# Optimization experiments

Hardware: AMD Instinct MI355X
Metric: run time of the kernel (lower is better)

Reference implementation:

```python
import jax, jax.numpy as jnp
import numpy as np

N, E, IN, H, C = 50000, 800000, 128, 256, 2
EPS = 1e-5


def setup_inputs() -> dict:
    key = jax.random.key(0)
    ks = jax.random.split(key, 12)
    inp = {
        "x": jax.random.normal(ks[0], (N, IN), jnp.float32),
        "edge_index": jax.random.randint(ks[1], (2, E), 0, N, jnp.int32),
        "w_nei0": jax.random.normal(ks[2], (IN, H), jnp.float32) * 0.05,
        "w_root0": jax.random.normal(ks[3], (IN, H), jnp.float32) * 0.05,
        "b0": jnp.zeros((H,), jnp.float32),
        "w_nei": jax.random.normal(ks[4], (2, H, H), jnp.float32) * 0.05,
        "w_root": jax.random.normal(ks[5], (2, H, H), jnp.float32) * 0.05,
        "b": jnp.zeros((2, H), jnp.float32),
        "bn_gamma": jnp.ones((3, H), jnp.float32),
        "bn_beta": jnp.zeros((3, H), jnp.float32),
        "bn_mean": jax.random.normal(ks[6], (3, H), jnp.float32) * 0.05,
        "bn_var": jnp.ones((3, H), jnp.float32),
        "w1": jax.random.normal(ks[7], (H, H // 2), jnp.float32) * 0.05,
        "b1": jnp.zeros((H // 2,), jnp.float32),
        "w2": jax.random.normal(ks[8], (H // 2, C), jnp.float32) * 0.05,
        "b2": jnp.zeros((C,), jnp.float32),
    }
    return inp


def _mean_aggregate(h, src, dst, inv_deg):
    # gather source-node features, scatter-sum to destinations, divide by degree
    agg = jax.ops.segment_sum(h[src], dst, num_segments=N)  # (N, d)
    return agg * inv_deg[:, None]


def _forward(x, edge_index, w_nei0, w_root0, b0, w_nei, w_root, b,
             bn_gamma, bn_beta, bn_mean, bn_var, w1, b1, w2, b2):
    src, dst = edge_index[0], edge_index[1]
    deg = jax.ops.segment_sum(jnp.ones((E,), x.dtype), dst, num_segments=N)
    inv_deg = 1.0 / jnp.maximum(deg, 1.0)

    h = x
    wn_list = [w_nei0, w_nei[0], w_nei[1]]
    wr_list = [w_root0, w_root[0], w_root[1]]
    bias_list = [b0, b[0], b[1]]
    for i in range(3):
        mean_nb = _mean_aggregate(h, src, dst, inv_deg)          # (N, d_in)
        h = mean_nb @ wn_list[i] + bias_list[i] + h @ wr_list[i]  # SAGEConv
        # BatchNorm1d (eval: running stats) + ReLU; dropout is identity in eval
        h = (h - bn_mean[i]) * jax.lax.rsqrt(bn_var[i] + EPS) * bn_gamma[i] + bn_beta[i]
        h = jax.nn.relu(h)

    h = jax.nn.relu(h @ w1 + b1)
    logits = h @ w2 + b2
    return jax.nn.log_softmax(logits, axis=1)


def reference(x, edge_index, w_nei0, w_root0, b0, w_nei, w_root, b,
              bn_gamma, bn_beta, bn_mean, bn_var, w1, b1, w2, b2):
    return _forward(x, edge_index, w_nei0, w_root0, b0, w_nei, w_root, b,
                    bn_gamma, bn_beta, bn_mean, bn_var, w1, b1, w2, b2)
```

## Files before the change

### kernel.cpp

```cpp
#include <hip/hip_runtime.h>
#include <hip/hip_fp16.h>

#define N_NODES 50000
#define N_EDGES 800000
#define DIM_IN 128
#define DIM_H 256

typedef _Float16 f16;
typedef _Float16 half8 __attribute__((ext_vector_type(8)));
typedef _Float16 f16x4 __attribute__((ext_vector_type(4)));
typedef _Float16 f16x2 __attribute__((ext_vector_type(2)));
typedef float f32x4 __attribute__((ext_vector_type(4)));
typedef unsigned int u32;

__device__ __forceinline__ void gload_lds16(const void* g, void* l) {
    __builtin_amdgcn_global_load_lds(
        (const __attribute__((address_space(1))) u32*)g,
        (__attribute__((address_space(3))) u32*)l,
        16, 0, 0);
}


__global__ void k_deg(const int* __restrict__ dst, int* __restrict__ deg) {
    int i = blockIdx.x * 256 + threadIdx.x;
    if (i < N_EDGES) atomicAdd(&deg[dst[i]], 1);
}

__global__ void k_scan1(const int* __restrict__ deg, int* __restrict__ row_start,
                        int* __restrict__ partials) {
    __shared__ int sm[256];
    int t = threadIdx.x;
    int i = blockIdx.x * 256 + t;
    int v = (i < N_NODES) ? deg[i] : 0;
    sm[t] = v;
    __syncthreads();
    for (int ofs = 1; ofs < 256; ofs <<= 1) {
        int add = (t >= ofs) ? sm[t - ofs] : 0;
        __syncthreads();
        sm[t] += add;
        __syncthreads();
    }
    if (i < N_NODES) row_start[i] = sm[t] - v;
    if (t == 255) partials[blockIdx.x] = sm[255];
}

__global__ void k_scan2(const int* __restrict__ partials, int* __restrict__ pscan, int nblk) {
    __shared__ int sm[256];
    int t = threadIdx.x;
    int v = (t < nblk) ? partials[t] : 0;
    sm[t] = v;
    __syncthreads();
    for (int ofs = 1; ofs < 256; ofs <<= 1) {
        int add = (t >= ofs) ? sm[t - ofs] : 0;
        __syncthreads();
        sm[t] += add;
        __syncthreads();
    }
    pscan[t] = sm[t] - v;
}

__global__ void k_scan3(const int* __restrict__ deg, int* __restrict__ row_start,
                        const int* __restrict__ pscan, float* __restrict__ inv_deg) {
    int i = blockIdx.x * 256 + threadIdx.x;
    if (i < N_NODES) {
        row_start[i] += pscan[blockIdx.x];
        int d = deg[i];
        inv_deg[i] = 1.0f / (float)(d > 1 ? d : 1);
        if (i == 0) row_start[N_NODES] = N_EDGES;
    }
}

__global__ void k_fill(const int* __restrict__ src, const int* __restrict__ dst,
                       const int* __restrict__ row_start, int* __restrict__ cursor,
                       int* __restrict__ csr) {
    int i = blockIdx.x * 256 + threadIdx.x;
    if (i < N_EDGES) {
        int d = dst[i];
        int p = atomicAdd(&cursor[d], 1);
        csr[row_start[d] + p] = src[i];
    }
}


__global__ void k_cvt_x(const float* __restrict__ x, f16* __restrict__ o) {
    int i = blockIdx.x * 256 + threadIdx.x;
    if (i < N_NODES * DIM_IN / 4) {
        float4 v = ((const float4*)x)[i];
        f16x4 h = {(f16)v.x, (f16)v.y, (f16)v.z, (f16)v.w};
        *(f16x4*)(o + (size_t)i * 4) = h;
    }
}

__global__ void k_tcvt(const float* __restrict__ W, f16* __restrict__ Wt, int K, int NN) {
    int t = blockIdx.x * 256 + threadIdx.x;
    if (t < K * NN) {
        int n = t / K, k = t - n * K;
        Wt[t] = (f16)W[(size_t)k * NN + n];
    }
}

__global__ void k_st(const float* __restrict__ b0, const float* __restrict__ bvec,
                     const float* __restrict__ gamma, const float* __restrict__ beta,
                     const float* __restrict__ mean, const float* __restrict__ var,
                     const float* __restrict__ b1, float* __restrict__ st) {
    int c = threadIdx.x;
    for (int layer = 0; layer < 3; layer++) {
        float bias = (layer == 0) ? b0[c] : bvec[(layer - 1) * DIM_H + c];
        float g = gamma[layer * DIM_H + c];
        float be = beta[layer * DIM_H + c];
        float mu = mean[layer * DIM_H + c];
        float va = var[layer * DIM_H + c];
        float s = g * rsqrtf(va + 1e-5f);
        st[layer * 512 + c] = s;
        st[layer * 512 + 256 + c] = (bias - mu) * s + be;
    }
    st[3 * 512 + c] = 1.0f;
    st[3 * 512 + 256 + c] = (c < 128) ? b1[c] : 0.0f;
}


template <int D>
__global__ void k_agg(const f16* __restrict__ h, const int* __restrict__ row_start,
                      const int* __restrict__ csr, const float* __restrict__ inv_deg,
                      f16* __restrict__ agg) {
    constexpr int V = D / 64;
    typedef _Float16 fvec __attribute__((ext_vector_type(V)));
    int wid = threadIdx.x >> 6;
    int lane = threadIdx.x & 63;
    int v = blockIdx.x * 4 + wid;
    if (v >= N_NODES) return;
    int e0 = row_start[v], e1 = row_start[v + 1];
    float acc[V];
#pragma unroll
    for (int j = 0; j < V; j++) acc[j] = 0.0f;

    const int li = lane & 15;
    for (int e = e0; e < e1; e += 16) {
        int ee = e + li;
        int idx = csr[ee < e1 ? ee : e1 - 1];
        int rem = e1 - e;
        fvec hv[16];
#pragma unroll
        for (int j = 0; j < 16; j++) {
            int s = __shfl(idx, j);
            hv[j] = *(const fvec*)(h + (size_t)s * D + lane * V);
        }
#pragma unroll
        for (int j = 0; j < 16; j++) {
            if (j < rem) {
#pragma unroll
                for (int q = 0; q < V; q++) acc[q] += (float)hv[j][q];
            }
        }
    }

    float sc = inv_deg[v];
    fvec o;
#pragma unroll
    for (int j = 0; j < V; j++) o[j] = (f16)(acc[j] * sc);
    *(fvec*)(agg + (size_t)v * D + lane * V) = o;
}


__global__ __launch_bounds__(256) void k_gemm(
    const f16* __restrict__ A1, int lda1, const f16* __restrict__ B1, int k1,
    const f16* __restrict__ A2, int lda2, const f16* __restrict__ B2, int k2,
    const float* __restrict__ sc, const float* __restrict__ sh,
    f16* __restrict__ out, int ldo, int M) {
    __shared__ f16 aT[128 * 32];
    __shared__ f16 bT[128 * 32];
    const int tid = threadIdx.x;
    const int lane = tid & 63;
    const int wid = tid >> 6;
    const int wm = wid >> 1, wn = wid & 1;
    const int m0 = blockIdx.x * 128;
    const int n0 = blockIdx.y * 128;
    f32x4 acc[4][4] = {};

    const int srow = tid >> 2;
    const int schunk = (tid & 3) ^ ((tid >> 3) & 3);
    const int ktot = k1 + k2;

    for (int kk = 0; kk < ktot; kk += 32) {
        const f16 *Ap, *Bp;
        int lda, ldb, kloc;
        if (kk < k1) { Ap = A1; Bp = B1; lda = lda1; ldb = k1; kloc = kk; }
        else         { Ap = A2; Bp = B2; lda = lda2; ldb = k2; kloc = kk - k1; }
#pragma unroll
        for (int hh = 0; hh < 2; hh++) {
            int r = hh * 64 + srow;
            int gm = m0 + r;
            gm = gm < M ? gm : M - 1;
            gload_lds16(Ap + (size_t)gm * lda + kloc + schunk * 8,
                        (char*)aT + hh * 4096 + tid * 16);
            gload_lds16(Bp + (size_t)(n0 + r) * ldb + kloc + schunk * 8,
                        (char*)bT + hh * 4096 + tid * 16);
        }
        __syncthreads();
        half8 af[4], bf[4];
#pragma unroll
        for (int mi = 0; mi < 4; mi++) {
            int row = wm * 64 + mi * 16 + (lane & 15);
            int ch = (lane >> 4) ^ ((row >> 1) & 3);
            af[mi] = *(const half8*)((const char*)aT + row * 64 + ch * 16);
        }
#pragma unroll
        for (int ni = 0; ni < 4; ni++) {
            int row = wn * 64 + ni * 16 + (lane & 15);
            int ch = (lane >> 4) ^ ((row >> 1) & 3);
            bf[ni] = *(const half8*)((const char*)bT + row * 64 + ch * 16);
        }
#pragma unroll
        for (int mi = 0; mi < 4; mi++)
#pragma unroll
            for (int ni = 0; ni < 4; ni++)
                acc[mi][ni] = __builtin_amdgcn_mfma_f32_16x16x32_f16(af[mi], bf[ni],
                                                                     acc[mi][ni], 0, 0, 0);
        __syncthreads();
    }

#pragma unroll
    for (int mi = 0; mi < 4; mi++) {
#pragma unroll
        for (int ni = 0; ni < 4; ni++) {
            int gcol = n0 + wn * 64 + ni * 16 + (lane & 15);
            float s = sc[gcol], t = sh[gcol];
#pragma unroll
            for (int r = 0; r < 4; r++) {
                int grow = m0 + wm * 64 + mi * 16 + (lane >> 4) * 4 + r;
                if (grow < M) {
                    float val = fmaxf(acc[mi][ni][r] * s + t, 0.0f);
                    out[(size_t)grow * ldo + gcol] = (f16)val;
                }
            }
        }
    }
}


__global__ void k_head2(const f16* __restrict__ h4, const float* __restrict__ w2,
                        const float* __restrict__ b2, float* __restrict__ out) {
    int wid = threadIdx.x >> 6, lane = threadIdx.x & 63;
    int row = blockIdx.x * 4 + wid;
    if (row >= N_NODES) return;
    f16x2 hv = *(const f16x2*)(h4 + (size_t)row * 128 + lane * 2);
    float4 w = *(const float4*)(w2 + lane * 4);
    float p0 = (float)hv[0] * w.x + (float)hv[1] * w.z;
    float p1 = (float)hv[0] * w.y + (float)hv[1] * w.w;
    for (int o = 32; o > 0; o >>= 1) {
        p0 += __shfl_xor(p0, o);
        p1 += __shfl_xor(p1, o);
    }
    if (lane == 0) {
        float l0 = p0 + b2[0], l1 = p1 + b2[1];
        float m = fmaxf(l0, l1);
        float lse = m + logf(expf(l0 - m) + expf(l1 - m));
        out[(size_t)row * 2] = l0 - lse;
        out[(size_t)row * 2 + 1] = l1 - lse;
    }
}


extern "C" void kernel_launch(void* const* d_in, const int* in_sizes, int n_in,
                              void* d_out, int out_size, void* d_ws, size_t ws_size,
                              hipStream_t stream) {
    const float* x     = (const float*)d_in[0];
    const int*   ei    = (const int*)d_in[1];
    const float* wn0   = (const float*)d_in[2];
    const float* wr0   = (const float*)d_in[3];
    const float* b0    = (const float*)d_in[4];
    const float* wn12  = (const float*)d_in[5];
    const float* wr12  = (const float*)d_in[6];
    const float* bvec  = (const float*)d_in[7];
    const float* gamma = (const float*)d_in[8];
    const float* beta  = (const float*)d_in[9];
    const float* mean  = (const float*)d_in[10];
    const float* var   = (const float*)d_in[11];
    const float* w1    = (const float*)d_in[12];
    const float* b1    = (const float*)d_in[13];
    const float* w2    = (const float*)d_in[14];
    const float* b2    = (const float*)d_in[15];
    const int* srcv = ei;
    const int* dstv = ei + N_EDGES;

    char* p = (char*)d_ws;
    auto alloc = [&](size_t bytes) {
        char* r = p;
        p += (bytes + 255) & ~(size_t)255;
        return r;
    };
    int*   deg       = (int*)alloc((size_t)N_NODES * 4);
    int*   row_start = (int*)alloc((size_t)(N_NODES + 1) * 4);
    int*   cursor    = (int*)alloc((size_t)N_NODES * 4);
    float* inv_deg   = (float*)alloc((size_t)N_NODES * 4);
    int*   partials  = (int*)alloc(256 * 4);
    int*   pscan     = (int*)alloc(256 * 4);
    int*   csr       = (int*)alloc((size_t)N_EDGES * 4);
    f16*   Wn0t      = (f16*)alloc(128 * 256 * 2);
    f16*   Wr0t      = (f16*)alloc(128 * 256 * 2);
    f16*   Wn1t      = (f16*)alloc(256 * 256 * 2);
    f16*   Wr1t      = (f16*)alloc(256 * 256 * 2);
    f16*   Wn2t      = (f16*)alloc(256 * 256 * 2);
    f16*   Wr2t      = (f16*)alloc(256 * 256 * 2);
    f16*   W1t       = (f16*)alloc(256 * 128 * 2);
    float* st        = (float*)alloc(4 * 512 * 4);
    f16*   hA        = (f16*)alloc((size_t)N_NODES * 256 * 2);
    f16*   hB        = (f16*)alloc((size_t)N_NODES * 256 * 2);
    f16*   agg       = (f16*)alloc((size_t)N_NODES * 256 * 2);

    hipMemsetAsync(deg, 0, (size_t)N_NODES * 4, stream);
    hipMemsetAsync(cursor, 0, (size_t)N_NODES * 4, stream);

    const int EB = (N_EDGES + 255) / 256;
    const int NBLK = (N_NODES + 255) / 256;
    k_deg<<<EB, 256, 0, stream>>>(dstv, deg);
    k_scan1<<<NBLK, 256, 0, stream>>>(deg, row_start, partials);
    k_scan2<<<1, 256, 0, stream>>>(partials, pscan, NBLK);
    k_scan3<<<NBLK, 256, 0, stream>>>(deg, row_start, pscan, inv_deg);
    k_fill<<<EB, 256, 0, stream>>>(srcv, dstv, row_start, cursor, csr);

    k_cvt_x<<<(N_NODES * DIM_IN / 4 + 255) / 256, 256, 0, stream>>>(x, hA);
    k_tcvt<<<128, 256, 0, stream>>>(wn0, Wn0t, 128, 256);
    k_tcvt<<<128, 256, 0, stream>>>(wr0, Wr0t, 128, 256);
    k_tcvt<<<256, 256, 0, stream>>>(wn12, Wn1t, 256, 256);
    k_tcvt<<<256, 256, 0, stream>>>(wn12 + 65536, Wn2t, 256, 256);
    k_tcvt<<<256, 256, 0, stream>>>(wr12, Wr1t, 256, 256);
    k_tcvt<<<256, 256, 0, stream>>>(wr12 + 65536, Wr2t, 256, 256);
    k_tcvt<<<128, 256, 0, stream>>>(w1, W1t, 256, 128);
    k_st<<<1, 256, 0, stream>>>(b0, bvec, gamma, beta, mean, var, b1, st);

    const int AB = (N_NODES + 3) / 4;
    dim3 g2((N_NODES + 127) / 128, 2), g1((N_NODES + 127) / 128, 1);

    k_agg<128><<<AB, 256, 0, stream>>>(hA, row_start, csr, inv_deg, agg);
    k_gemm<<<g2, 256, 0, stream>>>(agg, 128, Wn0t, 128, hA, 128, Wr0t, 128,
                                   st + 0, st + 256, hB, 256, N_NODES);
    k_agg<256><<<AB, 256, 0, stream>>>(hB, row_start, csr, inv_deg, agg);
    k_gemm<<<g2, 256, 0, stream>>>(agg, 256, Wn1t, 256, hB, 256, Wr1t, 256,
                                   st + 512, st + 768, hA, 256, N_NODES);
    k_agg<256><<<AB, 256, 0, stream>>>(hA, row_start, csr, inv_deg, agg);
    k_gemm<<<g2, 256, 0, stream>>>(agg, 256, Wn2t, 256, hA, 256, Wr2t, 256,
                                   st + 1024, st + 1280, hB, 256, N_NODES);
    k_gemm<<<g1, 256, 0, stream>>>(hB, 256, W1t, 256, (const f16*)nullptr, 0,
                                   (const f16*)nullptr, 0,
                                   st + 1536, st + 1792, agg, 128, N_NODES);
    k_head2<<<AB, 256, 0, stream>>>(agg, w2, b2, (float*)d_out);
}
```

Baseline: 398.1 us.

## Double-buffer GEMM LDS tiles, split 256-wide aggregation across waves, fuse MLP head

The GEMM kernel now double-buffers its LDS tiles so the global-to-LDS load of the next K slice is issued before the MFMAs on the current slice. The 256-dim aggregation now gives each node two waves, each loading half the row as 4-byte vectors, which doubles the waves available for the gather but re-reads the CSR indices twice. The final W1 GEMM is fused with the W2 projection and log-softmax, removing an intermediate write/read and one launch. Doubling LDS per block may reduce occupancy.

```diff
diff --git a/kernel.cpp b/kernel.cpp
--- a/kernel.cpp
+++ b/kernel.cpp
@@ -119,46 +119,71 @@
 }
 
 
-template <int D>
-__global__ void k_agg(const f16* __restrict__ h, const int* __restrict__ row_start,
-                      const int* __restrict__ csr, const float* __restrict__ inv_deg,
-                      f16* __restrict__ agg) {
-    constexpr int V = D / 64;
-    typedef _Float16 fvec __attribute__((ext_vector_type(V)));
+__global__ void k_agg128(const f16* __restrict__ h, const int* __restrict__ row_start,
+                         const int* __restrict__ csr, const float* __restrict__ inv_deg,
+                         f16* __restrict__ agg) {
     int wid = threadIdx.x >> 6;
     int lane = threadIdx.x & 63;
     int v = blockIdx.x * 4 + wid;
     if (v >= N_NODES) return;
     int e0 = row_start[v], e1 = row_start[v + 1];
-    float acc[V];
-#pragma unroll
-    for (int j = 0; j < V; j++) acc[j] = 0.0f;
+    float acc[2] = {0.0f, 0.0f};
 
     const int li = lane & 15;
     for (int e = e0; e < e1; e += 16) {
         int ee = e + li;
         int idx = csr[ee < e1 ? ee : e1 - 1];
         int rem = e1 - e;
-        fvec hv[16];
+        f16x2 hv[16];
 #pragma unroll
         for (int j = 0; j < 16; j++) {
             int s = __shfl(idx, j);
-            hv[j] = *(const fvec*)(h + (size_t)s * D + lane * V);
+            hv[j] = *(const f16x2*)(h + (size_t)s * 128 + lane * 2);
         }
 #pragma unroll
         for (int j = 0; j < 16; j++) {
-            if (j < rem) {
-#pragma unroll
-                for (int q = 0; q < V; q++) acc[q] += (float)hv[j][q];
-            }
+            if (j < rem) { acc[0] += (float)hv[j][0]; acc[1] += (float)hv[j][1]; }
         }
     }
 
     float sc = inv_deg[v];
-    fvec o;
-#pragma unroll
-    for (int j = 0; j < V; j++) o[j] = (f16)(acc[j] * sc);
-    *(fvec*)(agg + (size_t)v * D + lane * V) = o;
+    f16x2 o = {(f16)(acc[0] * sc), (f16)(acc[1] * sc)};
+    *(f16x2*)(agg + (size_t)v * 128 + lane * 2) = o;
+}
+
+
+__global__ void k_agg256(const f16* __restrict__ h, const int* __restrict__ row_start,
+                         const int* __restrict__ csr, const float* __restrict__ inv_deg,
+                         f16* __restrict__ agg) {
+    int wid = threadIdx.x >> 6;
+    int lane = threadIdx.x & 63;
+    int v = blockIdx.x * 2 + (wid >> 1);
+    int half = wid & 1;
+    if (v >= N_NODES) return;
+    int e0 = row_start[v], e1 = row_start[v + 1];
+    float acc[2] = {0.0f, 0.0f};
+
+    const f16* hb = h + half * 128 + lane * 2;
+    const int li = lane & 15;
+    for (int e = e0; e < e1; e += 16) {
+        int ee = e + li;
+        int idx = csr[ee < e1 ? ee : e1 - 1];
+        int rem = e1 - e;
+        f16x2 hv[16];
+#pragma unroll
+        for (int j = 0; j < 16; j++) {
+            int s = __shfl(idx, j);
+            hv[j] = *(const f16x2*)(hb + (size_t)s * 256);
+        }
+#pragma unroll
+        for (int j = 0; j < 16; j++) {
+            if (j < rem) { acc[0] += (float)hv[j][0]; acc[1] += (float)hv[j][1]; }
+        }
+    }
+
+    float sc = inv_deg[v];
+    f16x2 o = {(f16)(acc[0] * sc), (f16)(acc[1] * sc)};
+    *(f16x2*)(agg + (size_t)v * 256 + half * 128 + lane * 2) = o;
 }
 
 
@@ -167,8 +192,8 @@
     const f16* __restrict__ A2, int lda2, const f16* __restrict__ B2, int k2,
     const float* __restrict__ sc, const float* __restrict__ sh,
     f16* __restrict__ out, int ldo, int M) {
-    __shared__ f16 aT[128 * 32];
-    __shared__ f16 bT[128 * 32];
+    __shared__ f16 aT[2][128 * 32];
+    __shared__ f16 bT[2][128 * 32];
     const int tid = threadIdx.x;
     const int lane = tid & 63;
     const int wid = tid >> 6;
@@ -181,7 +206,7 @@
     const int schunk = (tid & 3) ^ ((tid >> 3) & 3);
     const int ktot = k1 + k2;
 
-    for (int kk = 0; kk < ktot; kk += 32) {
+    auto stage = [&](int buf, int kk) {
         const f16 *Ap, *Bp;
         int lda, ldb, kloc;
         if (kk < k1) { Ap = A1; Bp = B1; lda = lda1; ldb = k1; kloc = kk; }
@@ -192,23 +217,25 @@
             int gm = m0 + r;
             gm = gm < M ? gm : M - 1;
             gload_lds16(Ap + (size_t)gm * lda + kloc + schunk * 8,
-                        (char*)aT + hh * 4096 + tid * 16);
+                        (char*)&aT[buf][0] + hh * 4096 + tid * 16);
             gload_lds16(Bp + (size_t)(n0 + r) * ldb + kloc + schunk * 8,
-                        (char*)bT + hh * 4096 + tid * 16);
-        }
-        __syncthreads();
+                        (char*)&bT[buf][0] + hh * 4096 + tid * 16);
+        }
+    };
+
+    auto compute = [&](int buf) {
         half8 af[4], bf[4];
 #pragma unroll
         for (int mi = 0; mi < 4; mi++) {
             int row = wm * 64 + mi * 16 + (lane & 15);
             int ch = (lane >> 4) ^ ((row >> 1) & 3);
-            af[mi] = *(const half8*)((const char*)aT + row * 64 + ch * 16);
+            af[mi] = *(const half8*)((const char*)&aT[buf][0] + row * 64 + ch * 16);
         }
 #pragma unroll
         for (int ni = 0; ni < 4; ni++) {
             int row = wn * 64 + ni * 16 + (lane & 15);
             int ch = (lane >> 4) ^ ((row >> 1) & 3);
-            bf[ni] = *(const half8*)((const char*)bT + row * 64 + ch * 16);
+            bf[ni] = *(const half8*)((const char*)&bT[buf][0] + row * 64 + ch * 16);
         }
 #pragma unroll
         for (int mi = 0; mi < 4; mi++)
@@ -216,8 +243,18 @@
             for (int ni = 0; ni < 4; ni++)
                 acc[mi][ni] = __builtin_amdgcn_mfma_f32_16x16x32_f16(af[mi], bf[ni],
                                                                      acc[mi][ni], 0, 0, 0);
-        __syncthreads();
-    }
+    };
+
+    stage(0, 0);
+    __syncthreads();
+    int cur = 0;
+    for (int kk = 32; kk < ktot; kk += 32) {
+        stage(cur ^ 1, kk);
+        compute(cur);
+        __syncthreads();
+        cur ^= 1;
+    }
+    compute(cur);
 
 #pragma unroll
     for (int mi = 0; mi < 4; mi++) {
@@ -238,25 +275,112 @@
 }
 
 
-__global__ void k_head2(const f16* __restrict__ h4, const float* __restrict__ w2,
-                        const float* __restrict__ b2, float* __restrict__ out) {
-    int wid = threadIdx.x >> 6, lane = threadIdx.x & 63;
-    int row = blockIdx.x * 4 + wid;
-    if (row >= N_NODES) return;
-    f16x2 hv = *(const f16x2*)(h4 + (size_t)row * 128 + lane * 2);
-    float4 w = *(const float4*)(w2 + lane * 4);
-    float p0 = (float)hv[0] * w.x + (float)hv[1] * w.z;
-    float p1 = (float)hv[0] * w.y + (float)hv[1] * w.w;
-    for (int o = 32; o > 0; o >>= 1) {
-        p0 += __shfl_xor(p0, o);
-        p1 += __shfl_xor(p1, o);
-    }
-    if (lane == 0) {
-        float l0 = p0 + b2[0], l1 = p1 + b2[1];
-        float m = fmaxf(l0, l1);
-        float lse = m + logf(expf(l0 - m) + expf(l1 - m));
-        out[(size_t)row * 2] = l0 - lse;
-        out[(size_t)row * 2 + 1] = l1 - lse;
+__global__ __launch_bounds__(256) void k_gemm_head(
+    const f16* __restrict__ A1, int k1, const f16* __restrict__ B1,
+    const float* __restrict__ sh,
+    const float* __restrict__ w2, const float* __restrict__ b2,
+    float* __restrict__ out, int M) {
+    __shared__ f16 aT[2][128 * 32];
+    __shared__ f16 bT[2][128 * 32];
+    __shared__ float smred[128][2][2];
+    const int tid = threadIdx.x;
+    const int lane = tid & 63;
+    const int wid = tid >> 6;
+    const int wm = wid >> 1, wn = wid & 1;
+    const int m0 = blockIdx.x * 128;
+    f32x4 acc[4][4] = {};
+
+    const int srow = tid >> 2;
+    const int schunk = (tid & 3) ^ ((tid >> 3) & 3);
+
+    auto stage = [&](int buf, int kk) {
+#pragma unroll
+        for (int hh = 0; hh < 2; hh++) {
+            int r = hh * 64 + srow;
+            int gm = m0 + r;
+            gm = gm < M ? gm : M - 1;
+            gload_lds16(A1 + (size_t)gm * k1 + kk + schunk * 8,
+                        (char*)&aT[buf][0] + hh * 4096 + tid * 16);
+            gload_lds16(B1 + (size_t)r * k1 + kk + schunk * 8,
+                        (char*)&bT[buf][0] + hh * 4096 + tid * 16);
+        }
+    };
+
+    auto compute = [&](int buf) {
+        half8 af[4], bf[4];
+#pragma unroll
+        for (int mi = 0; mi < 4; mi++) {
+            int row = wm * 64 + mi * 16 + (lane & 15);
+            int ch = (lane >> 4) ^ ((row >> 1) & 3);
+            af[mi] = *(const half8*)((const char*)&aT[buf][0] + row * 64 + ch * 16);
+        }
+#pragma unroll
+        for (int ni = 0; ni < 4; ni++) {
+            int row = wn * 64 + ni * 16 + (lane & 15);
+            int ch = (lane >> 4) ^ ((row >> 1) & 3);
+            bf[ni] = *(const half8*)((const char*)&bT[buf][0] + row * 64 + ch * 16);
+        }
+#pragma unroll
+        for (int mi = 0; mi < 4; mi++)
+#pragma unroll
+            for (int ni = 0; ni < 4; ni++)
+                acc[mi][ni] = __builtin_amdgcn_mfma_f32_16x16x32_f16(af[mi], bf[ni],
+                                                                     acc[mi][ni], 0, 0, 0);
+    };
+
+    stage(0, 0);
+    __syncthreads();
+    int cur = 0;
+    for (int kk = 32; kk < k1; kk += 32) {
+        stage(cur ^ 1, kk);
+        compute(cur);
+        __syncthreads();
+        cur ^= 1;
+    }
+    compute(cur);
+
+    float w2c[4][2], shc[4];
+#pragma unroll
+    for (int ni = 0; ni < 4; ni++) {
+        int c = wn * 64 + ni * 16 + (lane & 15);
+        w2c[ni][0] = w2[c * 2];
+        w2c[ni][1] = w2[c * 2 + 1];
+        shc[ni] = sh[c];
+    }
+#pragma unroll
+    for (int mi = 0; mi < 4; mi++) {
+#pragma unroll
+        for (int r = 0; r < 4; r++) {
+            float p0 = 0.0f, p1 = 0.0f;
+#pragma unroll
+            for (int ni = 0; ni < 4; ni++) {
+                float val = fmaxf(acc[mi][ni][r] + shc[ni], 0.0f);
+                p0 += val * w2c[ni][0];
+                p1 += val * w2c[ni][1];
+            }
+#pragma unroll
+            for (int o = 1; o < 16; o <<= 1) {
+                p0 += __shfl_xor(p0, o);
+                p1 += __shfl_xor(p1, o);
+            }
+            if ((lane & 15) == 0) {
+                int lrow = wm * 64 + mi * 16 + (lane >> 4) * 4 + r;
+                smred[lrow][wn][0] = p0;
+                smred[lrow][wn][1] = p1;
+            }
+        }
+    }
+    __syncthreads();
+    if (tid < 128) {
+        int grow = m0 + tid;
+        if (grow < M) {
+            float l0 = smred[tid][0][0] + smred[tid][1][0] + b2[0];
+            float l1 = smred[tid][0][1] + smred[tid][1][1] + b2[1];
+            float m = fmaxf(l0, l1);
+            float lse = m + logf(expf(l0 - m) + expf(l1 - m));
+            out[(size_t)grow * 2] = l0 - lse;
+            out[(size_t)grow * 2 + 1] = l1 - lse;
+        }
     }
 }
 
@@ -329,20 +453,19 @@
     k_tcvt<<<128, 256, 0, stream>>>(w1, W1t, 256, 128);
     k_st<<<1, 256, 0, stream>>>(b0, bvec, gamma, beta, mean, var, b1, st);
 
-    const int AB = (N_NODES + 3) / 4;
-    dim3 g2((N_NODES + 127) / 128, 2), g1((N_NODES + 127) / 128, 1);
-
-    k_agg<128><<<AB, 256, 0, stream>>>(hA, row_start, csr, inv_deg, agg);
+    const int AB4 = (N_NODES + 3) / 4;
+    const int AB2 = (N_NODES + 1) / 2;
+    dim3 g2((N_NODES + 127) / 128, 2);
+
+    k_agg128<<<AB4, 256, 0, stream>>>(hA, row_start, csr, inv_deg, agg);
     k_gemm<<<g2, 256, 0, stream>>>(agg, 128, Wn0t, 128, hA, 128, Wr0t, 128,
                                    st + 0, st + 256, hB, 256, N_NODES);
-    k_agg<256><<<AB, 256, 0, stream>>>(hB, row_start, csr, inv_deg, agg);
+    k_agg256<<<AB2, 256, 0, stream>>>(hB, row_start, csr, inv_deg, agg);
     k_gemm<<<g2, 256, 0, stream>>>(agg, 256, Wn1t, 256, hB, 256, Wr1t, 256,
                                    st + 512, st + 768, hA, 256, N_NODES);
-    k_agg<256><<<AB, 256, 0, stream>>>(hA, row_start, csr, inv_deg, agg);
+    k_agg256<<<AB2, 256, 0, stream>>>(hA, row_start, csr, inv_deg, agg);
     k_gemm<<<g2, 256, 0, stream>>>(agg, 256, Wn2t, 256, hA, 256, Wr2t, 256,
                                    st + 1024, st + 1280, hB, 256, N_NODES);
-    k_gemm<<<g1, 256, 0, stream>>>(hB, 256, W1t, 256, (const f16*)nullptr, 0,
-                                   (const f16*)nullptr, 0,
-                                   st + 1536, st + 1792, agg, 128, N_NODES);
-    k_head2<<<AB, 256, 0, stream>>>(agg, w2, b2, (float*)d_out);
-}
+    k_gemm_head<<<(N_NODES + 127) / 128, 256, 0, stream>>>(
+        hB, 256, W1t, st + 1792, w2, b2, (float*)d_out, N_NODES);
+}
```

New measurement: 397.1 us. About the same (-0.3%).
